# Kernel optimization log

Hardware: AMD Instinct MI355X
Metric: run time of the kernel (lower is better)

Reference implementation:

```python
import jax, jax.numpy as jnp
import numpy as np

N, E, D = 100000, 1600000, 64
L = 3          # num_layers
EPS = 1e-5     # LayerNorm eps


def setup_inputs() -> dict:
    key = jax.random.key(0)
    ks = jax.random.split(key, 8)
    s = 0.05
    return {
        "x": jax.random.normal(ks[0], (N, D), jnp.float32),
        "edge_src": jax.random.randint(ks[1], (E,), 0, N, jnp.int32),
        "edge_dst": jax.random.randint(ks[2], (E,), 0, N, jnp.int32),
        # SAGEConv: lin_l (on aggregated neighbors, with bias), lin_r (root, no bias)
        "w_l": (jax.random.normal(ks[3], (L, D, D)) * s).astype(jnp.float32),
        "b_l": jnp.zeros((L, D), jnp.float32),
        "w_r": (jax.random.normal(ks[4], (L, D, D)) * s).astype(jnp.float32),
        # LayerNorm affine params per layer
        "gamma": jnp.ones((L, D), jnp.float32),
        "beta": jnp.zeros((L, D), jnp.float32),
        # residual projection (layer 0 only; Identity afterwards)
        "w_res": (jax.random.normal(ks[5], (D, D)) * s).astype(jnp.float32),
        "b_res": jnp.zeros((D,), jnp.float32),
        # final fc
        "w_fc": (jax.random.normal(ks[6], (D, D)) * s).astype(jnp.float32),
        "b_fc": jnp.zeros((D,), jnp.float32),
    }


def _layer_norm(h, g, b):
    mu = jnp.mean(h, axis=-1, keepdims=True)
    var = jnp.var(h, axis=-1, keepdims=True)
    return (h - mu) * jax.lax.rsqrt(var + EPS) * g + b


def reference(x, edge_src, edge_dst, w_l, b_l, w_r, gamma, beta, w_res, b_res, w_fc, b_fc):
    n = x.shape[0]
    # in-degree for mean aggregation (nodes with no in-edges get 0 aggregate)
    deg = jax.ops.segment_sum(jnp.ones(edge_dst.shape, x.dtype), edge_dst, num_segments=n)
    inv_deg = jnp.where(deg > 0, 1.0 / jnp.maximum(deg, 1.0), 0.0)[:, None]  # [N,1]
    for i in range(L):
        residual = x @ w_res + b_res if i == 0 else x
        # SAGEConv mean aggregation: gather source feats, scatter-sum at dst, divide by degree
        agg = jax.ops.segment_sum(x[edge_src], edge_dst, num_segments=n) * inv_deg  # [N,D]
        h = agg @ w_l[i] + b_l[i] + x @ w_r[i]
        h = jax.nn.relu(_layer_norm(h, gamma[i], beta[i]))
        # dropout is inactive in eval mode
        x = h + residual
    return x @ w_fc + b_fc
```

## Files before the change

kernel.cpp:

```cpp
#include <hip/hip_runtime.h>

typedef unsigned short u16;
typedef __bf16 bf16x8 __attribute__((ext_vector_type(8)));
typedef float f32x4 __attribute__((ext_vector_type(4)));

#define D 64
#define LPITCH 136
#define CHUNKS 256
#define BSHIFT 9
#define CCAP 1280

__device__ __forceinline__ float b2f(u16 u) {
    unsigned v = ((unsigned)u) << 16;
    float f;
    __builtin_memcpy(&f, &v, 4);
    return f;
}
__device__ __forceinline__ float u2f_lo(unsigned u) {
    unsigned v = u << 16;
    float f;
    __builtin_memcpy(&f, &v, 4);
    return f;
}
__device__ __forceinline__ float u2f_hi(unsigned u) {
    unsigned v = u & 0xFFFF0000u;
    float f;
    __builtin_memcpy(&f, &v, 4);
    return f;
}
__device__ __forceinline__ u16 f2b(float f) {
    unsigned u;
    __builtin_memcpy(&u, &f, 4);
    u = u + 0x7FFFu + ((u >> 16) & 1u);
    return (u16)(u >> 16);
}
__device__ __forceinline__ bf16x8 ld_frag(const u16* p) {
    union { uint4 u; bf16x8 b; } cv;
    cv.u = *(const uint4*)p;
    return cv.b;
}

__global__ __launch_bounds__(256) void binA_kernel(const int* __restrict__ dst, int E,
                                                   int* __restrict__ H, int nbuck, int eper,
                                                   const float* __restrict__ xf,
                                                   u16* __restrict__ xb, int total4,
                                                   const float* __restrict__ wl,
                                                   const float* __restrict__ wr,
                                                   const float* __restrict__ wres,
                                                   const float* __restrict__ wfc,
                                                   u16* __restrict__ WtL,
                                                   u16* __restrict__ WresT,
                                                   u16* __restrict__ WfcT,
                                                   int* __restrict__ row_ptr, int N) {
    __shared__ int hist[256];
    int t = threadIdx.x;
    int c = blockIdx.x;
    hist[t] = 0;
    __syncthreads();
    {
        int beg = c * eper, end = min(beg + eper, E);
        for (int i = beg + t; i < end; i += 256)
            atomicAdd(&hist[dst[i] >> BSHIFT], 1);
    }
    __syncthreads();
    if (t < nbuck) H[c * nbuck + t] = hist[t];

    int gid = c * 256 + t;
    int gstr = CHUNKS * 256;
    if (gid == 0) row_ptr[N] = E;
    for (int i = gid; i < total4; i += gstr) {
        float4 v = *(const float4*)(xf + i * 4);
        ushort4 o;
        o.x = f2b(v.x); o.y = f2b(v.y); o.z = f2b(v.z); o.w = f2b(v.w);
        *(ushort4*)(xb + i * 4) = o;
    }
    for (int idx = gid; idx < 3 * 64 * 128; idx += gstr) {
        int l = idx >> 13;
        int rem = idx & 8191;
        int n = rem >> 7;
        int k = rem & 127;
        float v = (k < 64) ? wl[l * 4096 + k * 64 + n] : wr[l * 4096 + (k - 64) * 64 + n];
        WtL[idx] = f2b(v);
    }
    for (int idx = gid; idx < 4096; idx += gstr) {
        int n = idx >> 6, k = idx & 63;
        WresT[idx] = f2b(wres[k * 64 + n]);
        WfcT[idx] = f2b(wfc[k * 64 + n]);
    }
}

__global__ __launch_bounds__(256) void binS2_kernel(const int* __restrict__ H,
                                                    int* __restrict__ Orel,
                                                    int* __restrict__ T,
                                                    int nbuck) {
    __shared__ int ss[256];
    int b = blockIdx.x;
    int t = threadIdx.x;
    int h = H[t * nbuck + b];
    ss[t] = h;
    __syncthreads();
    for (int off = 1; off < 256; off <<= 1) {
        int v = (t >= off) ? ss[t - off] : 0;
        __syncthreads();
        ss[t] += v;
        __syncthreads();
    }
    Orel[t * nbuck + b] = ss[t] - h;
    if (t == 255) T[b] = ss[255];
}

__global__ __launch_bounds__(256) void binB_kernel(const int* __restrict__ src,
                                                   const int* __restrict__ dst, int E,
                                                   const int* __restrict__ T,
                                                   const int* __restrict__ Orel,
                                                   int* __restrict__ staging,
                                                   int nbuck, int eper) {
    __shared__ int sc[256];
    int t = threadIdx.x;
    int c = blockIdx.x;
    int v = (t < nbuck) ? T[t] : 0;
    sc[t] = v;
    __syncthreads();
    for (int off = 1; off < 256; off <<= 1) {
        int u = (t >= off) ? sc[t - off] : 0;
        __syncthreads();
        sc[t] += u;
        __syncthreads();
    }
    int baseT = sc[t] - v;
    int porel = (t < nbuck) ? Orel[c * nbuck + t] : 0;
    __syncthreads();
    sc[t] = baseT + porel;
    __syncthreads();
    int beg = c * eper, end = min(beg + eper, E);
    const int mask = (1 << BSHIFT) - 1;
    for (int i = beg + t; i < end; i += 256) {
        int d = dst[i];
        int b = d >> BSHIFT;
        int p = atomicAdd(&sc[b], 1);
        staging[p] = src[i] | ((d & mask) << 17);
    }
}

__global__ __launch_bounds__(256) void binC_kernel(const int* __restrict__ staging,
                                                   const int* __restrict__ T,
                                                   int* __restrict__ row_ptr,
                                                   float* __restrict__ inv_deg,
                                                   int* __restrict__ col, int N, int nbuck) {
    __shared__ int cnt[512];
    __shared__ int lrp[512];
    __shared__ int sm[256];
    __shared__ int span[2];
    int b = blockIdx.x;
    int t = threadIdx.x;
    int v = (t < nbuck) ? T[t] : 0;
    sm[t] = v;
    __syncthreads();
    for (int off = 1; off < 256; off <<= 1) {
        int u = (t >= off) ? sm[t - off] : 0;
        __syncthreads();
        sm[t] += u;
        __syncthreads();
    }
    if (t == b) { span[0] = sm[t] - v; span[1] = sm[t]; }
    cnt[t] = 0;
    cnt[t + 256] = 0;
    __syncthreads();
    int sbeg = span[0], send = span[1];
    int node0 = b << BSHIFT;
    int nn = min(1 << BSHIFT, N - node0);
    for (int i = sbeg + t; i < send; i += 256)
        atomicAdd(&cnt[staging[i] >> 17], 1);
    __syncthreads();
    int c0 = cnt[2 * t], c1 = cnt[2 * t + 1];
    sm[t] = c0 + c1;
    __syncthreads();
    for (int off = 1; off < 256; off <<= 1) {
        int u = (t >= off) ? sm[t - off] : 0;
        __syncthreads();
        sm[t] += u;
        __syncthreads();
    }
    int excl = sm[t] - c0 - c1;
    lrp[2 * t] = excl;
    lrp[2 * t + 1] = excl + c0;
    __syncthreads();
    for (int i = t; i < nn; i += 256) {
        row_ptr[node0 + i] = sbeg + lrp[i];
        int dd = cnt[i];
        inv_deg[node0 + i] = dd > 0 ? 1.0f / (float)dd : 0.0f;
    }
    __syncthreads();
    for (int i = sbeg + t; i < send; i += 256) {
        int word = staging[i];
        int ld = word >> 17;
        int k = atomicSub(&cnt[ld], 1) - 1;
        col[sbeg + lrp[ld] + k] = word & 0x1FFFF;
    }
}

__global__ __launch_bounds__(256, 4) void layer_kernel(const u16* __restrict__ xb_in,
                                                       const int* __restrict__ row_ptr,
                                                       const int* __restrict__ col,
                                                       const float* __restrict__ inv_deg,
                                                       const u16* __restrict__ Wt,
                                                       const float* __restrict__ bl,
                                                       const float* __restrict__ gam,
                                                       const float* __restrict__ bet,
                                                       const u16* __restrict__ WresT,
                                                       const float* __restrict__ bres,
                                                       const u16* __restrict__ WfcT,
                                                       const float* __restrict__ bfc,
                                                       u16* __restrict__ xb_out,
                                                       float* __restrict__ fout,
                                                       int N, int layer0, int final_) {
    __shared__ __align__(16) u16 sA[64 * LPITCH];
    __shared__ __align__(16) u16 sB[64 * LPITCH];
    __shared__ int lcol[CCAP];
    __shared__ int rp[65];
    __shared__ float ideg[64];
    int tid = threadIdx.x;
    int base = blockIdx.x * 64;
    int lane = tid & 63;
    int w = tid >> 6;

#pragma unroll
    for (int i = 0; i < 4; i++) {
        int idx = i * 256 + tid;
        int r = idx >> 4, c = idx & 15;
        *(uint4*)&sB[r * LPITCH + c * 8] = *(const uint4*)(Wt + idx * 8);
    }
#pragma unroll
    for (int i = 0; i < 2; i++) {
        int idx = i * 256 + tid;
        int r = idx >> 3, c = idx & 7;
        int node = base + r;
        uint4 v = make_uint4(0, 0, 0, 0);
        if (node < N) v = *(const uint4*)(xb_in + node * D + c * 8);
        *(uint4*)&sA[r * LPITCH + 64 + c * 8] = v;
    }
    if (tid < 65) rp[tid] = row_ptr[min(base + tid, N)];
    if (tid < 64) ideg[tid] = (base + tid < N) ? inv_deg[base + tid] : 0.f;
    __syncthreads();

    int e0 = rp[0];
    int tileE = rp[64] - e0;
    bool fits = tileE <= CCAP;
    if (fits) {
        for (int i = tid; i < tileE; i += 256) lcol[i] = col[e0 + i];
    }
    __syncthreads();

    int slot = lane >> 3;
    int chunk = lane & 7;
    auto run_gather = [&](auto LD) {
#pragma unroll
        for (int r = 0; r < 2; r++) {
            int node_l = w * 16 + r * 8 + slot;
            float a0 = 0, a1 = 0, a2 = 0, a3 = 0, a4 = 0, a5 = 0, a6 = 0, a7 = 0;
            int e = rp[node_l], end = rp[node_l + 1];
#define ACC(v)                                          \
    a0 += u2f_lo(v.x); a1 += u2f_hi(v.x);               \
    a2 += u2f_lo(v.y); a3 += u2f_hi(v.y);               \
    a4 += u2f_lo(v.z); a5 += u2f_hi(v.z);               \
    a6 += u2f_lo(v.w); a7 += u2f_hi(v.w);
            for (; e + 7 < end; e += 8) {
                int s0 = LD(e),     s1 = LD(e + 1), s2 = LD(e + 2), s3 = LD(e + 3);
                int s4 = LD(e + 4), s5 = LD(e + 5), s6 = LD(e + 6), s7 = LD(e + 7);
                uint4 v0 = *(const uint4*)(xb_in + s0 * D + chunk * 8);
                uint4 v1 = *(const uint4*)(xb_in + s1 * D + chunk * 8);
                uint4 v2 = *(const uint4*)(xb_in + s2 * D + chunk * 8);
                uint4 v3 = *(const uint4*)(xb_in + s3 * D + chunk * 8);
                uint4 v4 = *(const uint4*)(xb_in + s4 * D + chunk * 8);
                uint4 v5 = *(const uint4*)(xb_in + s5 * D + chunk * 8);
                uint4 v6 = *(const uint4*)(xb_in + s6 * D + chunk * 8);
                uint4 v7 = *(const uint4*)(xb_in + s7 * D + chunk * 8);
                ACC(v0) ACC(v1) ACC(v2) ACC(v3)
                ACC(v4) ACC(v5) ACC(v6) ACC(v7)
            }
            if (e + 3 < end) {
                int s0 = LD(e), s1 = LD(e + 1), s2 = LD(e + 2), s3 = LD(e + 3);
                uint4 v0 = *(const uint4*)(xb_in + s0 * D + chunk * 8);
                uint4 v1 = *(const uint4*)(xb_in + s1 * D + chunk * 8);
                uint4 v2 = *(const uint4*)(xb_in + s2 * D + chunk * 8);
                uint4 v3 = *(const uint4*)(xb_in + s3 * D + chunk * 8);
                ACC(v0) ACC(v1) ACC(v2) ACC(v3)
                e += 4;
            }
            if (e + 1 < end) {
                int s0 = LD(e), s1 = LD(e + 1);
                uint4 v0 = *(const uint4*)(xb_in + s0 * D + chunk * 8);
                uint4 v1 = *(const uint4*)(xb_in + s1 * D + chunk * 8);
                ACC(v0) ACC(v1)
                e += 2;
            }
            if (e < end) {
                int s0 = LD(e);
                uint4 v0 = *(const uint4*)(xb_in + s0 * D + chunk * 8);
                ACC(v0)
            }
#undef ACC
            float m = ideg[node_l];
            uint4 o;
            o.x = (unsigned)f2b(a0 * m) | ((unsigned)f2b(a1 * m) << 16);
            o.y = (unsigned)f2b(a2 * m) | ((unsigned)f2b(a3 * m) << 16);
            o.z = (unsigned)f2b(a4 * m) | ((unsigned)f2b(a5 * m) << 16);
            o.w = (unsigned)f2b(a6 * m) | ((unsigned)f2b(a7 * m) << 16);
            *(uint4*)&sA[node_l * LPITCH + chunk * 8] = o;
        }
    };
    if (fits) run_gather([&](int e) { return lcol[e - e0]; });
    else      run_gather([&](int e) { return col[e]; });
    __syncthreads();

    int q = lane >> 4;
    int ln = lane & 15;
    f32x4 acc[4] = {{0, 0, 0, 0}, {0, 0, 0, 0}, {0, 0, 0, 0}, {0, 0, 0, 0}};
    f32x4 accr[4] = {{0, 0, 0, 0}, {0, 0, 0, 0}, {0, 0, 0, 0}, {0, 0, 0, 0}};
    const u16* aRow = &sA[(w * 16 + ln) * LPITCH];

#pragma unroll
    for (int c = 0; c < 4; c++) {
        bf16x8 a = ld_frag(&aRow[c * 32 + q * 8]);
#pragma unroll
        for (int t = 0; t < 4; t++) {
            bf16x8 b = ld_frag(&sB[(t * 16 + ln) * LPITCH + c * 32 + q * 8]);
            acc[t] = __builtin_amdgcn_mfma_f32_16x16x32_bf16(a, b, acc[t], 0, 0, 0);
        }
    }
    if (layer0) {
#pragma unroll
        for (int c = 0; c < 2; c++) {
            bf16x8 a = ld_frag(&aRow[64 + c * 32 + q * 8]);
#pragma unroll
            for (int t = 0; t < 4; t++) {
                bf16x8 b = ld_frag(WresT + (t * 16 + ln) * 64 + c * 32 + q * 8);
                accr[t] = __builtin_amdgcn_mfma_f32_16x16x32_bf16(a, b, accr[t], 0, 0, 0);
            }
        }
    }

    float bcol[4], gcol[4], btcol[4], brcol[4];
#pragma unroll
    for (int t = 0; t < 4; t++) {
        int colI = t * 16 + ln;
        bcol[t] = bl[colI];
        gcol[t] = gam[colI];
        btcol[t] = bet[colI];
        brcol[t] = layer0 ? bres[colI] : 0.f;
    }
#pragma unroll
    for (int t = 0; t < 4; t++)
#pragma unroll
        for (int r = 0; r < 4; r++) acc[t][r] += bcol[t];

    float ps[4], pq[4];
#pragma unroll
    for (int r = 0; r < 4; r++) {
        float s = 0, s2 = 0;
#pragma unroll
        for (int t = 0; t < 4; t++) { float h = acc[t][r]; s += h; s2 += h * h; }
        ps[r] = s; pq[r] = s2;
    }
    for (int off = 1; off < 16; off <<= 1) {
#pragma unroll
        for (int r = 0; r < 4; r++) {
            ps[r] += __shfl_xor(ps[r], off, 64);
            pq[r] += __shfl_xor(pq[r], off, 64);
        }
    }
#pragma unroll
    for (int r = 0; r < 4; r++) {
        int nb = w * 16 + q * 4 + r;
        float mu = ps[r] * (1.f / 64.f);
        float var = pq[r] * (1.f / 64.f) - mu * mu;
        var = var < 0.f ? 0.f : var;
        float rstd = rsqrtf(var + 1e-5f);
#pragma unroll
        for (int t = 0; t < 4; t++) {
            int colI = t * 16 + ln;
            float hn = (acc[t][r] - mu) * rstd * gcol[t] + btcol[t];
            hn = hn > 0.f ? hn : 0.f;
            float res = layer0 ? (accr[t][r] + brcol[t])
                               : b2f(sA[nb * LPITCH + 64 + colI]);
            sA[nb * LPITCH + colI] = f2b(hn + res);
        }
    }

    if (final_) {
        f32x4 accf[4] = {{0, 0, 0, 0}, {0, 0, 0, 0}, {0, 0, 0, 0}, {0, 0, 0, 0}};
#pragma unroll
        for (int c = 0; c < 2; c++) {
            bf16x8 a = ld_frag(&aRow[c * 32 + q * 8]);
#pragma unroll
            for (int t = 0; t < 4; t++) {
                bf16x8 b = ld_frag(WfcT + (t * 16 + ln) * 64 + c * 32 + q * 8);
                accf[t] = __builtin_amdgcn_mfma_f32_16x16x32_bf16(a, b, accf[t], 0, 0, 0);
            }
        }
        __syncthreads();
        float* fB = (float*)sB;
#pragma unroll
        for (int r = 0; r < 4; r++) {
            int nb = w * 16 + q * 4 + r;
#pragma unroll
            for (int t = 0; t < 4; t++) {
                int colI = t * 16 + ln;
                fB[nb * 68 + colI] = accf[t][r] + bfc[colI];
            }
        }
        __syncthreads();
#pragma unroll
        for (int i = 0; i < 4; i++) {
            int idx = i * 256 + tid;
            int row = idx >> 4, cc = idx & 15;
            int node = base + row;
            if (node < N)
                *(float4*)(fout + node * D + cc * 4) = *(const float4*)&fB[row * 68 + cc * 4];
        }
    } else {
#pragma unroll
        for (int i = 0; i < 2; i++) {
            int idx = i * 64 + lane;
            int row = w * 16 + (idx >> 3);
            int ch = idx & 7;
            int node = base + row;
            if (node < N)
                *(uint4*)(xb_out + node * D + ch * 8) = *(const uint4*)&sA[row * LPITCH + ch * 8];
        }
    }
}

extern "C" void kernel_launch(void* const* d_in, const int* in_sizes, int n_in,
                              void* d_out, int out_size, void* d_ws, size_t ws_size,
                              hipStream_t stream) {
    const float* x_in = (const float*)d_in[0];
    const int* e_src = (const int*)d_in[1];
    const int* e_dst = (const int*)d_in[2];
    const float* w_l = (const float*)d_in[3];
    const float* b_l = (const float*)d_in[4];
    const float* w_r = (const float*)d_in[5];
    const float* gam = (const float*)d_in[6];
    const float* bet = (const float*)d_in[7];
    const float* w_res = (const float*)d_in[8];
    const float* b_res = (const float*)d_in[9];
    const float* w_fc = (const float*)d_in[10];
    const float* b_fc = (const float*)d_in[11];
    float* out = (float*)d_out;

    const int N = in_sizes[0] / D;
    const int E = in_sizes[1];
    const int nbuck = ((N - 1) >> BSHIFT) + 1;
    const int eper = (E + CHUNKS - 1) / CHUNKS;

    size_t o = 0;
    auto carve = [&](size_t bytes) {
        size_t cur = o;
        o += (bytes + 255) & ~(size_t)255;
        return (char*)d_ws + cur;
    };
    int* row_ptr = (int*)carve((size_t)(N + 1) * 4);
    float* inv_deg = (float*)carve((size_t)N * 4);
    int* colA = (int*)carve((size_t)E * 4);
    int* staging = (int*)carve((size_t)E * 4);
    int* Hh = (int*)carve((size_t)CHUNKS * nbuck * 4);
    int* Orel = (int*)carve((size_t)CHUNKS * nbuck * 4);
    int* Tb = (int*)carve((size_t)nbuck * 4);
    u16* WtL = (u16*)carve(3 * 64 * 128 * 2);
    u16* WresT = (u16*)carve(64 * 64 * 2);
    u16* WfcT = (u16*)carve(64 * 64 * 2);
    u16* xbA = (u16*)carve((size_t)N * D * 2);
    u16* xbB = (u16*)carve((size_t)N * D * 2);

    binA_kernel<<<CHUNKS, 256, 0, stream>>>(e_dst, E, Hh, nbuck, eper,
                                            x_in, xbA, N * D / 4,
                                            w_l, w_r, w_res, w_fc, WtL, WresT, WfcT,
                                            row_ptr, N);
    binS2_kernel<<<nbuck, 256, 0, stream>>>(Hh, Orel, Tb, nbuck);
    binB_kernel<<<CHUNKS, 256, 0, stream>>>(e_src, e_dst, E, Tb, Orel, staging,
                                            nbuck, eper);
    binC_kernel<<<nbuck, 256, 0, stream>>>(staging, Tb, row_ptr, inv_deg, colA, N, nbuck);

    int gridT = (N + 63) / 64;

    layer_kernel<<<gridT, 256, 0, stream>>>(xbA, row_ptr, colA, inv_deg, WtL,
                                            b_l, gam, bet, WresT, b_res,
                                            WfcT, b_fc, xbB, out, N, 1, 0);
    layer_kernel<<<gridT, 256, 0, stream>>>(xbB, row_ptr, colA, inv_deg, WtL + 8192,
                                            b_l + 64, gam + 64, bet + 64, WresT, b_res,
                                            WfcT, b_fc, xbA, out, N, 0, 0);
    layer_kernel<<<gridT, 256, 0, stream>>>(xbA, row_ptr, colA, inv_deg, WtL + 16384,
                                            b_l + 128, gam + 128, bet + 128, WresT, b_res,
                                            WfcT, b_fc, xbB, out, N, 0, 1);
}
```

Before: 281.1 us.

## Split bf16 features into four column planes and drop separate scan kernel

Node features are stored as four 16-column bf16 planes (32 bytes per node per plane) instead of row-major 128-byte rows. The gather now walks each plane in turn, with 4 lanes splitting a node's edges and shuffle-reducing, so each plane's working set is smaller and more likely to stay in cache. It also removes the binS2 prefix-scan kernel: binB and binC recompute the bucket totals and per-chunk offsets directly from the histogram. The trade-off is four passes over the edge list per node, extra shuffles, and each binB/binC block re-reading the full 256×nbuck histogram.

```diff
diff --git a/kernel.cpp b/kernel.cpp
--- a/kernel.cpp
+++ b/kernel.cpp
@@ -43,7 +43,7 @@
 __global__ __launch_bounds__(256) void binA_kernel(const int* __restrict__ dst, int E,
                                                    int* __restrict__ H, int nbuck, int eper,
                                                    const float* __restrict__ xf,
-                                                   u16* __restrict__ xb, int total4,
+                                                   u16* __restrict__ xb, int N, int N16,
                                                    const float* __restrict__ wl,
                                                    const float* __restrict__ wr,
                                                    const float* __restrict__ wres,
@@ -51,7 +51,7 @@
                                                    u16* __restrict__ WtL,
                                                    u16* __restrict__ WresT,
                                                    u16* __restrict__ WfcT,
-                                                   int* __restrict__ row_ptr, int N) {
+                                                   int* __restrict__ row_ptr) {
     __shared__ int hist[256];
     int t = threadIdx.x;
     int c = blockIdx.x;
@@ -68,11 +68,18 @@
     int gid = c * 256 + t;
     int gstr = CHUNKS * 256;
     if (gid == 0) row_ptr[N] = E;
-    for (int i = gid; i < total4; i += gstr) {
-        float4 v = *(const float4*)(xf + i * 4);
-        ushort4 o;
-        o.x = f2b(v.x); o.y = f2b(v.y); o.z = f2b(v.z); o.w = f2b(v.w);
-        *(ushort4*)(xb + i * 4) = o;
+    int nchunks = N * 8;
+    for (int i = gid; i < nchunks; i += gstr) {
+        int node = i >> 3, ch = i & 7;
+        const float* s = xf + node * 64 + ch * 8;
+        float4 v0 = *(const float4*)s;
+        float4 v1 = *(const float4*)(s + 4);
+        uint4 o;
+        o.x = (unsigned)f2b(v0.x) | ((unsigned)f2b(v0.y) << 16);
+        o.y = (unsigned)f2b(v0.z) | ((unsigned)f2b(v0.w) << 16);
+        o.z = (unsigned)f2b(v1.x) | ((unsigned)f2b(v1.y) << 16);
+        o.w = (unsigned)f2b(v1.z) | ((unsigned)f2b(v1.w) << 16);
+        *(uint4*)(xb + (size_t)(ch >> 1) * N16 + node * 16 + (ch & 1) * 8) = o;
     }
     for (int idx = gid; idx < 3 * 64 * 128; idx += gstr) {
         int l = idx >> 13;
@@ -89,37 +96,21 @@
     }
 }
 
-__global__ __launch_bounds__(256) void binS2_kernel(const int* __restrict__ H,
-                                                    int* __restrict__ Orel,
-                                                    int* __restrict__ T,
-                                                    int nbuck) {
-    __shared__ int ss[256];
-    int b = blockIdx.x;
-    int t = threadIdx.x;
-    int h = H[t * nbuck + b];
-    ss[t] = h;
-    __syncthreads();
-    for (int off = 1; off < 256; off <<= 1) {
-        int v = (t >= off) ? ss[t - off] : 0;
-        __syncthreads();
-        ss[t] += v;
-        __syncthreads();
-    }
-    Orel[t * nbuck + b] = ss[t] - h;
-    if (t == 255) T[b] = ss[255];
-}
-
 __global__ __launch_bounds__(256) void binB_kernel(const int* __restrict__ src,
                                                    const int* __restrict__ dst, int E,
-                                                   const int* __restrict__ T,
-                                                   const int* __restrict__ Orel,
+                                                   const int* __restrict__ H,
                                                    int* __restrict__ staging,
                                                    int nbuck, int eper) {
     __shared__ int sc[256];
     int t = threadIdx.x;
     int c = blockIdx.x;
-    int v = (t < nbuck) ? T[t] : 0;
-    sc[t] = v;
+    int pre = 0, tot = 0;
+    for (int cc = 0; cc < CHUNKS; cc++) {
+        int h = (t < nbuck) ? H[cc * nbuck + t] : 0;
+        if (cc < c) pre += h;
+        tot += h;
+    }
+    sc[t] = tot;
     __syncthreads();
     for (int off = 1; off < 256; off <<= 1) {
         int u = (t >= off) ? sc[t - off] : 0;
@@ -127,10 +118,9 @@
         sc[t] += u;
         __syncthreads();
     }
-    int baseT = sc[t] - v;
-    int porel = (t < nbuck) ? Orel[c * nbuck + t] : 0;
-    __syncthreads();
-    sc[t] = baseT + porel;
+    int baseT = sc[t] - tot;
+    __syncthreads();
+    sc[t] = baseT + pre;
     __syncthreads();
     int beg = c * eper, end = min(beg + eper, E);
     const int mask = (1 << BSHIFT) - 1;
@@ -143,7 +133,7 @@
 }
 
 __global__ __launch_bounds__(256) void binC_kernel(const int* __restrict__ staging,
-                                                   const int* __restrict__ T,
+                                                   const int* __restrict__ H,
                                                    int* __restrict__ row_ptr,
                                                    float* __restrict__ inv_deg,
                                                    int* __restrict__ col, int N, int nbuck) {
@@ -153,8 +143,10 @@
     __shared__ int span[2];
     int b = blockIdx.x;
     int t = threadIdx.x;
-    int v = (t < nbuck) ? T[t] : 0;
-    sm[t] = v;
+    int tot = 0;
+    for (int cc = 0; cc < CHUNKS; cc++)
+        tot += (t < nbuck) ? H[cc * nbuck + t] : 0;
+    sm[t] = tot;
     __syncthreads();
     for (int off = 1; off < 256; off <<= 1) {
         int u = (t >= off) ? sm[t - off] : 0;
@@ -162,7 +154,7 @@
         sm[t] += u;
         __syncthreads();
     }
-    if (t == b) { span[0] = sm[t] - v; span[1] = sm[t]; }
+    if (t == b) { span[0] = sm[t] - tot; span[1] = sm[t]; }
     cnt[t] = 0;
     cnt[t + 256] = 0;
     __syncthreads();
@@ -213,7 +205,7 @@
                                                        const float* __restrict__ bfc,
                                                        u16* __restrict__ xb_out,
                                                        float* __restrict__ fout,
-                                                       int N, int layer0, int final_) {
+                                                       int N, int N16, int layer0, int final_) {
     __shared__ __align__(16) u16 sA[64 * LPITCH];
     __shared__ __align__(16) u16 sB[64 * LPITCH];
     __shared__ int lcol[CCAP];
@@ -236,7 +228,8 @@
         int r = idx >> 3, c = idx & 7;
         int node = base + r;
         uint4 v = make_uint4(0, 0, 0, 0);
-        if (node < N) v = *(const uint4*)(xb_in + node * D + c * 8);
+        if (node < N)
+            v = *(const uint4*)(xb_in + (size_t)(c >> 1) * N16 + node * 16 + (c & 1) * 8);
         *(uint4*)&sA[r * LPITCH + 64 + c * 8] = v;
     }
     if (tid < 65) rp[tid] = row_ptr[min(base + tid, N)];
@@ -252,61 +245,55 @@
     __syncthreads();
 
     int slot = lane >> 3;
-    int chunk = lane & 7;
+    int j = lane & 7;
+    int es = j >> 1;
+    int h = j & 1;
     auto run_gather = [&](auto LD) {
 #pragma unroll
         for (int r = 0; r < 2; r++) {
             int node_l = w * 16 + r * 8 + slot;
-            float a0 = 0, a1 = 0, a2 = 0, a3 = 0, a4 = 0, a5 = 0, a6 = 0, a7 = 0;
-            int e = rp[node_l], end = rp[node_l + 1];
+            int beg = rp[node_l], end = rp[node_l + 1];
+            float m = ideg[node_l];
+#pragma unroll
+            for (int p = 0; p < 4; p++) {
+                const u16* tab = xb_in + (size_t)p * N16 + h * 8;
+                float a0 = 0, a1 = 0, a2 = 0, a3 = 0, a4 = 0, a5 = 0, a6 = 0, a7 = 0;
 #define ACC(v)                                          \
     a0 += u2f_lo(v.x); a1 += u2f_hi(v.x);               \
     a2 += u2f_lo(v.y); a3 += u2f_hi(v.y);               \
     a4 += u2f_lo(v.z); a5 += u2f_hi(v.z);               \
     a6 += u2f_lo(v.w); a7 += u2f_hi(v.w);
-            for (; e + 7 < end; e += 8) {
-                int s0 = LD(e),     s1 = LD(e + 1), s2 = LD(e + 2), s3 = LD(e + 3);
-                int s4 = LD(e + 4), s5 = LD(e + 5), s6 = LD(e + 6), s7 = LD(e + 7);
-                uint4 v0 = *(const uint4*)(xb_in + s0 * D + chunk * 8);
-                uint4 v1 = *(const uint4*)(xb_in + s1 * D + chunk * 8);
-                uint4 v2 = *(const uint4*)(xb_in + s2 * D + chunk * 8);
-                uint4 v3 = *(const uint4*)(xb_in + s3 * D + chunk * 8);
-                uint4 v4 = *(const uint4*)(xb_in + s4 * D + chunk * 8);
-                uint4 v5 = *(const uint4*)(xb_in + s5 * D + chunk * 8);
-                uint4 v6 = *(const uint4*)(xb_in + s6 * D + chunk * 8);
-                uint4 v7 = *(const uint4*)(xb_in + s7 * D + chunk * 8);
-                ACC(v0) ACC(v1) ACC(v2) ACC(v3)
-                ACC(v4) ACC(v5) ACC(v6) ACC(v7)
+                int e = beg + es;
+                for (; e + 12 < end; e += 16) {
+                    int s0 = LD(e), s1 = LD(e + 4), s2 = LD(e + 8), s3 = LD(e + 12);
+                    uint4 v0 = *(const uint4*)(tab + s0 * 16);
+                    uint4 v1 = *(const uint4*)(tab + s1 * 16);
+                    uint4 v2 = *(const uint4*)(tab + s2 * 16);
+                    uint4 v3 = *(const uint4*)(tab + s3 * 16);
+                    ACC(v0) ACC(v1) ACC(v2) ACC(v3)
+                }
+                for (; e < end; e += 4) {
+                    int s0 = LD(e);
+                    uint4 v0 = *(const uint4*)(tab + s0 * 16);
+                    ACC(v0)
+                }
+#undef ACC
+                a0 += __shfl_xor(a0, 2, 64); a0 += __shfl_xor(a0, 4, 64);
+                a1 += __shfl_xor(a1, 2, 64); a1 += __shfl_xor(a1, 4, 64);
+                a2 += __shfl_xor(a2, 2, 64); a2 += __shfl_xor(a2, 4, 64);
+                a3 += __shfl_xor(a3, 2, 64); a3 += __shfl_xor(a3, 4, 64);
+                a4 += __shfl_xor(a4, 2, 64); a4 += __shfl_xor(a4, 4, 64);
+                a5 += __shfl_xor(a5, 2, 64); a5 += __shfl_xor(a5, 4, 64);
+                a6 += __shfl_xor(a6, 2, 64); a6 += __shfl_xor(a6, 4, 64);
+                a7 += __shfl_xor(a7, 2, 64); a7 += __shfl_xor(a7, 4, 64);
+                uint4 o;
+                o.x = (unsigned)f2b(a0 * m) | ((unsigned)f2b(a1 * m) << 16);
+                o.y = (unsigned)f2b(a2 * m) | ((unsigned)f2b(a3 * m) << 16);
+                o.z = (unsigned)f2b(a4 * m) | ((unsigned)f2b(a5 * m) << 16);
+                o.w = (unsigned)f2b(a6 * m) | ((unsigned)f2b(a7 * m) << 16);
+                if (es == 0)
+                    *(uint4*)&sA[node_l * LPITCH + p * 16 + h * 8] = o;
             }
-            if (e + 3 < end) {
-                int s0 = LD(e), s1 = LD(e + 1), s2 = LD(e + 2), s3 = LD(e + 3);
-                uint4 v0 = *(const uint4*)(xb_in + s0 * D + chunk * 8);
-                uint4 v1 = *(const uint4*)(xb_in + s1 * D + chunk * 8);
-                uint4 v2 = *(const uint4*)(xb_in + s2 * D + chunk * 8);
-                uint4 v3 = *(const uint4*)(xb_in + s3 * D + chunk * 8);
-                ACC(v0) ACC(v1) ACC(v2) ACC(v3)
-                e += 4;
-            }
-            if (e + 1 < end) {
-                int s0 = LD(e), s1 = LD(e + 1);
-                uint4 v0 = *(const uint4*)(xb_in + s0 * D + chunk * 8);
-                uint4 v1 = *(const uint4*)(xb_in + s1 * D + chunk * 8);
-                ACC(v0) ACC(v1)
-                e += 2;
-            }
-            if (e < end) {
-                int s0 = LD(e);
-                uint4 v0 = *(const uint4*)(xb_in + s0 * D + chunk * 8);
-                ACC(v0)
-            }
-#undef ACC
-            float m = ideg[node_l];
-            uint4 o;
-            o.x = (unsigned)f2b(a0 * m) | ((unsigned)f2b(a1 * m) << 16);
-            o.y = (unsigned)f2b(a2 * m) | ((unsigned)f2b(a3 * m) << 16);
-            o.z = (unsigned)f2b(a4 * m) | ((unsigned)f2b(a5 * m) << 16);
-            o.w = (unsigned)f2b(a6 * m) | ((unsigned)f2b(a7 * m) << 16);
-            *(uint4*)&sA[node_l * LPITCH + chunk * 8] = o;
         }
     };
     if (fits) run_gather([&](int e) { return lcol[e - e0]; });
@@ -359,7 +346,7 @@
     for (int r = 0; r < 4; r++) {
         float s = 0, s2 = 0;
 #pragma unroll
-        for (int t = 0; t < 4; t++) { float h = acc[t][r]; s += h; s2 += h * h; }
+        for (int t = 0; t < 4; t++) { float hh = acc[t][r]; s += hh; s2 += hh * hh; }
         ps[r] = s; pq[r] = s2;
     }
     for (int off = 1; off < 16; off <<= 1) {
@@ -426,7 +413,8 @@
             int ch = idx & 7;
             int node = base + row;
             if (node < N)
-                *(uint4*)(xb_out + node * D + ch * 8) = *(const uint4*)&sA[row * LPITCH + ch * 8];
+                *(uint4*)(xb_out + (size_t)(ch >> 1) * N16 + node * 16 + (ch & 1) * 8) =
+                    *(const uint4*)&sA[row * LPITCH + ch * 8];
         }
     }
 }
@@ -450,6 +438,7 @@
 
     const int N = in_sizes[0] / D;
     const int E = in_sizes[1];
+    const int N16 = N * 16;
     const int nbuck = ((N - 1) >> BSHIFT) + 1;
     const int eper = (E + CHUNKS - 1) / CHUNKS;
 
@@ -464,8 +453,6 @@
     int* colA = (int*)carve((size_t)E * 4);
     int* staging = (int*)carve((size_t)E * 4);
     int* Hh = (int*)carve((size_t)CHUNKS * nbuck * 4);
-    int* Orel = (int*)carve((size_t)CHUNKS * nbuck * 4);
-    int* Tb = (int*)carve((size_t)nbuck * 4);
     u16* WtL = (u16*)carve(3 * 64 * 128 * 2);
     u16* WresT = (u16*)carve(64 * 64 * 2);
     u16* WfcT = (u16*)carve(64 * 64 * 2);
@@ -473,23 +460,21 @@
     u16* xbB = (u16*)carve((size_t)N * D * 2);
 
     binA_kernel<<<CHUNKS, 256, 0, stream>>>(e_dst, E, Hh, nbuck, eper,
-                                            x_in, xbA, N * D / 4,
+                                            x_in, xbA, N, N16,
                                             w_l, w_r, w_res, w_fc, WtL, WresT, WfcT,
-                                            row_ptr, N);
-    binS2_kernel<<<nbuck, 256, 0, stream>>>(Hh, Orel, Tb, nbuck);
-    binB_kernel<<<CHUNKS, 256, 0, stream>>>(e_src, e_dst, E, Tb, Orel, staging,
-                                            nbuck, eper);
-    binC_kernel<<<nbuck, 256, 0, stream>>>(staging, Tb, row_ptr, inv_deg, colA, N, nbuck);
+                                            row_ptr);
+    binB_kernel<<<CHUNKS, 256, 0, stream>>>(e_src, e_dst, E, Hh, staging, nbuck, eper);
+    binC_kernel<<<nbuck, 256, 0, stream>>>(staging, Hh, row_ptr, inv_deg, colA, N, nbuck);
 
     int gridT = (N + 63) / 64;
 
     layer_kernel<<<gridT, 256, 0, stream>>>(xbA, row_ptr, colA, inv_deg, WtL,
                                             b_l, gam, bet, WresT, b_res,
-                                            WfcT, b_fc, xbB, out, N, 1, 0);
+                                            WfcT, b_fc, xbB, out, N, N16, 1, 0);
     layer_kernel<<<gridT, 256, 0, stream>>>(xbB, row_ptr, colA, inv_deg, WtL + 8192,
                                             b_l + 64, gam + 64, bet + 64, WresT, b_res,
-                                            WfcT, b_fc, xbA, out, N, 0, 0);
+                                            WfcT, b_fc, xbA, out, N, N16, 0, 0);
     layer_kernel<<<gridT, 256, 0, stream>>>(xbA, row_ptr, colA, inv_deg, WtL + 16384,
                                             b_l + 128, gam + 128, bet + 128, WresT, b_res,
-                                            WfcT, b_fc, xbB, out, N, 0, 1);
-}
+                                            WfcT, b_fc, xbB, out, N, N16, 0, 1);
+}
```

Measured after the change: 405.4 us. 1.44x slower.
